# Kernel tuning notes

Measured on AMD Instinct MI355X. Metric: run time of the kernel, lower is better.

The kernel has to match this reference:

```python
import jax, jax.numpy as jnp
import numpy as np

N_EMBD = 1024
N_HEAD = 16
HEAD_DIM = N_EMBD // N_HEAD
B, S = 4, 1024


def setup_inputs() -> dict:
    key = jax.random.key(0)
    k1, k2, k3 = jax.random.split(key, 3)
    scale = 0.02
    return {
        "x": jax.random.normal(k1, (B, S, N_EMBD), dtype=jnp.float32),
        "Wqkv": jax.random.normal(k2, (N_EMBD, 3 * N_EMBD), dtype=jnp.float32) * scale,
        "bqkv": jnp.zeros((3 * N_EMBD,), dtype=jnp.float32),
        "Wproj": jax.random.normal(k3, (N_EMBD, N_EMBD), dtype=jnp.float32) * scale,
        "bproj": jnp.zeros((N_EMBD,), dtype=jnp.float32),
    }


def reference(x, Wqkv, bqkv, Wproj, bproj):
    b, s, e = x.shape
    qkv = x @ Wqkv + bqkv  # (b, s, 3e)
    q, k, v = jnp.split(qkv, 3, axis=-1)
    # (b, h, s, d)
    q = q.reshape(b, s, N_HEAD, HEAD_DIM).transpose(0, 2, 1, 3)
    k = k.reshape(b, s, N_HEAD, HEAD_DIM).transpose(0, 2, 1, 3)
    v = v.reshape(b, s, N_HEAD, HEAD_DIM).transpose(0, 2, 1, 3)
    scores = jnp.einsum("bhqd,bhkd->bhqk", q, k) / jnp.sqrt(
        jnp.asarray(HEAD_DIM, dtype=x.dtype)
    )
    causal = jnp.tril(jnp.ones((s, s), dtype=bool))  # (s, s)
    scores = jnp.where(causal[None, None, :, :], scores, jnp.asarray(-jnp.inf, dtype=scores.dtype))
    attn = jax.nn.softmax(scores, axis=-1)
    out = jnp.einsum("bhqk,bhkd->bhqd", attn, v)
    out = out.transpose(0, 2, 1, 3).reshape(b, s, e)
    return out @ Wproj + bproj
```

## Files before the change

### kernel.cpp

```cpp
#include <hip/hip_runtime.h>

#define S_LEN 1024
#define EMB   1024
#define NH    16
#define HD    64
#define BATCH 4
#define M_TOT 4096
#define QSZ   (BATCH * NH * S_LEN * HD)

typedef __attribute__((ext_vector_type(4))) float  f32x4;
typedef __attribute__((ext_vector_type(8))) __bf16 bf16x8;

__device__ __forceinline__ unsigned short f2bf(float f) {
  union { float f; unsigned u; } a; a.f = f;
  unsigned r = a.u + 0x7fffu + ((a.u >> 16) & 1u);
  return (unsigned short)(r >> 16);
}

__device__ __forceinline__ float fexp2(float x) {
#if __has_builtin(__builtin_amdgcn_exp2f)
  return __builtin_amdgcn_exp2f(x);
#else
  return exp2f(x);
#endif
}

__global__ void cvt_bf16(const float4* __restrict__ in, ushort4* __restrict__ out, int n4) {
  int i = blockIdx.x * blockDim.x + threadIdx.x;
  if (i >= n4) return;
  float4 v = in[i];
  ushort4 o;
  o.x = f2bf(v.x); o.y = f2bf(v.y); o.z = f2bf(v.z); o.w = f2bf(v.w);
  out[i] = o;
}

__global__ void cvt_transpose(const float* __restrict__ in, unsigned short* __restrict__ out,
                              int K, int N) {
  __shared__ unsigned short tile[32][33];
  int n0 = blockIdx.x * 32, k0 = blockIdx.y * 32;
  int tx = threadIdx.x, ty = threadIdx.y;
  #pragma unroll
  for (int r = ty; r < 32; r += 8)
    tile[r][tx] = f2bf(in[(size_t)(k0 + r) * N + n0 + tx]);
  __syncthreads();
  #pragma unroll
  for (int r = ty; r < 32; r += 8)
    out[(size_t)(n0 + r) * K + k0 + tx] = tile[tx][r];
}

template<int EPI>
__global__ __launch_bounds__(512, 4) void gemm_tile(
    const unsigned short* __restrict__ A,
    const unsigned short* __restrict__ Bt,
    const float* __restrict__ bias,
    void* __restrict__ outp,
    int K, int Nout)
{
  __shared__ alignas(16) char smem[65536];
  const int m0 = blockIdx.x * 128, n0 = blockIdx.y * 128;
  const int t = threadIdx.x;
  const int wid = t >> 6, lane = t & 63;
  const int wm = wid >> 2, wn = wid & 3;
  const int lr = lane & 15, lg = lane >> 4;
  const int nkt = K >> 6;

  f32x4 acc[4][2] = {};

  auto STAGE = [&](int b, int kt) {
    const int k0 = kt << 6;
    #pragma unroll
    for (int l = 0; l < 2; ++l) {
      const int L = l * 8192 + t * 16;
      const int row = L >> 7, c = (L >> 4) & 7;
      const int ce = (c ^ (row & 7)) << 3;
      const unsigned short* gA = A  + (size_t)(m0 + row) * K + k0 + ce;
      const unsigned short* gB = Bt + (size_t)(n0 + row) * K + k0 + ce;
      __builtin_amdgcn_global_load_lds(
          (const __attribute__((address_space(1))) unsigned int*)gA,
          (__attribute__((address_space(3))) unsigned int*)(smem + b * 32768 + L),
          16, 0, 0);
      __builtin_amdgcn_global_load_lds(
          (const __attribute__((address_space(1))) unsigned int*)gB,
          (__attribute__((address_space(3))) unsigned int*)(smem + b * 32768 + 16384 + L),
          16, 0, 0);
    }
  };

  STAGE(0, 0);

  for (int kt = 0; kt < nkt; ++kt) {
    const int cur = kt & 1;
    if (kt + 1 < nkt) {
      STAGE(cur ^ 1, kt + 1);
      asm volatile("s_waitcnt vmcnt(4)" ::: "memory");
    } else {
      asm volatile("s_waitcnt vmcnt(0)" ::: "memory");
    }
    __builtin_amdgcn_s_barrier();
    asm volatile("" ::: "memory");

    const char* Ab = smem + cur * 32768;
    const char* Bb = Ab + 16384;
    bf16x8 af[4][2], bfr[2][2];
    #pragma unroll
    for (int i = 0; i < 4; ++i)
      #pragma unroll
      for (int kk = 0; kk < 2; ++kk) {
        const int row = wm * 64 + i * 16 + lr;
        af[i][kk] = *(const bf16x8*)(Ab + row * 128 + (((kk * 4 + lg) ^ (row & 7)) << 4));
      }
    #pragma unroll
    for (int j = 0; j < 2; ++j)
      #pragma unroll
      for (int kk = 0; kk < 2; ++kk) {
        const int row = wn * 32 + j * 16 + lr;
        bfr[j][kk] = *(const bf16x8*)(Bb + row * 128 + (((kk * 4 + lg) ^ (row & 7)) << 4));
      }
    __builtin_amdgcn_s_setprio(1);
    #pragma unroll
    for (int i = 0; i < 4; ++i)
      #pragma unroll
      for (int j = 0; j < 2; ++j)
        #pragma unroll
        for (int kk = 0; kk < 2; ++kk)
          acc[i][j] = __builtin_amdgcn_mfma_f32_16x16x32_bf16(af[i][kk], bfr[j][kk], acc[i][j], 0, 0, 0);
    __builtin_amdgcn_s_setprio(0);

    asm volatile("s_waitcnt lgkmcnt(0)" ::: "memory");
    __builtin_amdgcn_s_barrier();
  }

  if (EPI == 0) {
    unsigned short* O = (unsigned short*)outp;
    const int sec = n0 >> 10;
    if (sec < 2) {
      #pragma unroll
      for (int i = 0; i < 4; ++i)
        #pragma unroll
        for (int j = 0; j < 2; ++j) {
          const int col = n0 + wn * 32 + j * 16 + lr;
          const float bv = bias[col];
          const int cc = col & 1023, h = cc >> 6, d = cc & 63;
          #pragma unroll
          for (int r = 0; r < 4; ++r) {
            const int row = m0 + wm * 64 + i * 16 + lg * 4 + r;
            float v = acc[i][j][r] + bv;
            if (sec == 0) v *= 0.18033688f;
            const int bb = row >> 10, ss = row & 1023;
            O[(size_t)sec * QSZ + (((size_t)(bb * NH + h) * S_LEN + ss) * HD + d)] = f2bf(v);
          }
        }
    } else {
      unsigned short* T = (unsigned short*)smem;
      #pragma unroll
      for (int i = 0; i < 4; ++i)
        #pragma unroll
        for (int j = 0; j < 2; ++j) {
          const int ci = wn * 32 + j * 16 + lr;
          const float bv = bias[n0 + ci];
          union { ushort4 s4; __bf16 b[4]; } pk;
          #pragma unroll
          for (int r = 0; r < 4; ++r) pk.b[r] = (__bf16)(acc[i][j][r] + bv);
          *(ushort4*)(T + ci * 136 + wm * 64 + i * 16 + lg * 4) = pk.s4;
        }
      __syncthreads();
      const int ci = t >> 2, part = t & 3;
      const int cc = (n0 - 2048) + ci;
      const int h = cc >> 6, d = cc & 63;
      const int bb2 = m0 >> 10, sbase = m0 & 1023;
      unsigned short* dst = O + 2ull * QSZ +
          ((size_t)(bb2 * NH + h) * HD + d) * S_LEN + sbase;
      #pragma unroll
      for (int u = 0; u < 4; ++u) {
        const int spos = part * 32 + u * 8;
        *(bf16x8*)(dst + spos) = *(const bf16x8*)(T + ci * 136 + spos);
      }
    }
  } else {
    float* Of = (float*)outp;
    #pragma unroll
    for (int i = 0; i < 4; ++i)
      #pragma unroll
      for (int j = 0; j < 2; ++j) {
        const int col = n0 + wn * 32 + j * 16 + lr;
        const float bv = bias[col];
        #pragma unroll
        for (int r = 0; r < 4; ++r) {
          const int row = m0 + wm * 64 + i * 16 + lg * 4 + r;
          Of[(size_t)row * (size_t)Nout + col] = acc[i][j][r] + bv;
        }
      }
  }
}

__device__ __forceinline__ void group_tile(
    const bf16x8 (&kf)[8], const bf16x8 (&vf)[8], const bf16x8 (&qf)[2],
    int kt, int q0, bool diag, int lr, int lg,
    float& m, float& lp, f32x4 (&o)[4])
{
  f32x4 sacc[4] = {};
  __builtin_amdgcn_s_setprio(1);
  #pragma unroll
  for (int nt = 0; nt < 4; ++nt)
    #pragma unroll
    for (int kk = 0; kk < 2; ++kk)
      sacc[nt] = __builtin_amdgcn_mfma_f32_16x16x32_bf16(kf[nt * 2 + kk], qf[kk], sacc[nt], 0, 0, 0);
  __builtin_amdgcn_s_setprio(0);

  float p[16];
  if (diag) {
    const int q = q0 + lr;
    #pragma unroll
    for (int nt = 0; nt < 4; ++nt)
      #pragma unroll
      for (int r = 0; r < 4; ++r) {
        int k = kt * 64 + nt * 16 + lg * 4 + r;
        p[nt * 4 + r] = (k > q) ? -1e30f : sacc[nt][r];
      }
  } else {
    #pragma unroll
    for (int nt = 0; nt < 4; ++nt)
      #pragma unroll
      for (int r = 0; r < 4; ++r)
        p[nt * 4 + r] = sacc[nt][r];
  }

  float r8[8], r4[4];
  #pragma unroll
  for (int i = 0; i < 8; ++i) r8[i] = fmaxf(p[i], p[i + 8]);
  #pragma unroll
  for (int i = 0; i < 4; ++i) r4[i] = fmaxf(r8[i], r8[i + 4]);
  float pm = fmaxf(fmaxf(r4[0], r4[1]), fmaxf(r4[2], r4[3]));
  if (__any(pm > m + 11.5f)) {
    float px = fmaxf(pm, __shfl_xor(pm, 16, 64));
    px = fmaxf(px, __shfl_xor(px, 32, 64));
    float mn = fmaxf(m, px);
    float fs = fexp2(m - mn);
    lp *= fs;
    #pragma unroll
    for (int dt = 0; dt < 4; ++dt)
      #pragma unroll
      for (int r = 0; r < 4; ++r) o[dt][r] *= fs;
    m = mn;
  }
  #pragma unroll
  for (int i = 0; i < 16; ++i) p[i] = fexp2(p[i] - m);

  float s8[8], s4[4];
  #pragma unroll
  for (int i = 0; i < 8; ++i) s8[i] = p[i] + p[i + 8];
  #pragma unroll
  for (int i = 0; i < 4; ++i) s4[i] = s8[i] + s8[i + 4];
  lp += (s4[0] + s4[1]) + (s4[2] + s4[3]);

  union { unsigned u[8]; __bf16 b[16]; } W;
  #pragma unroll
  for (int i = 0; i < 16; ++i) W.b[i] = (__bf16)p[i];

  const int dl0 = ((2 * (lg & 1) + (lg >> 1)) * 16 + lr) << 2;
  const int dl1 = ((2 * ((lg & 1) ^ 1) + (lg >> 1)) * 16 + lr) << 2;
  const bool oddlg = (lg & 1) != 0;
  const bool hb    = (lg >> 1) != 0;
  union { unsigned u[4]; bf16x8 v; } T0, T1;
  #pragma unroll
  for (int kk = 0; kk < 2; ++kk) {
    #pragma unroll
    for (int c = 0; c < 2; ++c) {
      unsigned vlo = W.u[4 * kk + c];
      unsigned vhi = W.u[4 * kk + 2 + c];
      unsigned s0 = oddlg ? vhi : vlo;
      unsigned s1 = oddlg ? vlo : vhi;
      unsigned r0 = (unsigned)__builtin_amdgcn_ds_permute(dl0, (int)s0);
      unsigned r1 = (unsigned)__builtin_amdgcn_ds_permute(dl1, (int)s1);
      unsigned* T = kk ? T1.u : T0.u;
      T[c]     = hb ? r1 : r0;
      T[2 + c] = hb ? r0 : r1;
    }
  }

  __builtin_amdgcn_s_setprio(1);
  #pragma unroll
  for (int dt = 0; dt < 4; ++dt) {
    o[dt] = __builtin_amdgcn_mfma_f32_16x16x32_bf16(vf[dt * 2 + 0], T0.v, o[dt], 0, 0, 0);
    o[dt] = __builtin_amdgcn_mfma_f32_16x16x32_bf16(vf[dt * 2 + 1], T1.v, o[dt], 0, 0, 0);
  }
  __builtin_amdgcn_s_setprio(0);
}

__device__ __forceinline__ void group_epilogue(
    const f32x4 (&o)[4], float lp, int q0, int lr, int lg,
    char* Ep, unsigned short* __restrict__ attout, int bb, int h)
{
  float l2 = lp + __shfl_xor(lp, 16, 64);
  float l4 = l2 + __shfl_xor(l2, 32, 64);
  float rl = 1.0f / l4;
  #pragma unroll
  for (int dt = 0; dt < 4; ++dt) {
    union { ushort4 s4; __bf16 b[4]; } ov;
    #pragma unroll
    for (int r = 0; r < 4; ++r) ov.b[r] = (__bf16)(o[dt][r] * rl);
    int byt = (lr * 128 + (dt * 16 + lg * 4) * 2) ^ ((lr & 7) << 4);
    *(ushort4*)(Ep + byt) = ov.s4;
  }
  asm volatile("s_waitcnt lgkmcnt(0)" ::: "memory");
  const int lane = lr + lg * 16;
  const int ql = lane >> 2, c = lane & 3;
  #pragma unroll
  for (int s = 0; s < 2; ++s) {
    int byt = (ql * 128 + (c * 16 + s * 8) * 2) ^ ((ql & 7) << 4);
    bf16x8 vrow = *(const bf16x8*)(Ep + byt);
    *(bf16x8*)(attout + (size_t)(bb * S_LEN + q0 + ql) * EMB + h * HD + c * 16 + s * 8) = vrow;
  }
}

__global__ __launch_bounds__(256, 2) void attn_fwd(
    const unsigned short* __restrict__ Q,
    const unsigned short* __restrict__ K,
    const unsigned short* __restrict__ Vt,
    unsigned short* __restrict__ attout)
{
  __shared__ alignas(16) char stage[2][16384];
  __shared__ alignas(16) char Ep_lds[4][2048];
  const int bid = blockIdx.x;
  const int bh   = ((bid & 7) << 3) | ((bid >> 3) & 7);
  const int base = bid >> 6;
  const int wv = threadIdx.x >> 6, lane = threadIdx.x & 63;
  const int pi = base * 4 + wv;
  const int lr = lane & 15, lg = lane >> 4;
  const int nkt  = 16 - base;
  const int nktl = base + 1;
  const int q0h = (63 - pi) * 16, q0l = pi * 16;
  const unsigned short* Qb = Q  + (size_t)bh * (S_LEN * HD);
  const unsigned short* Kh = K  + (size_t)bh * (S_LEN * HD);
  const unsigned short* Vh = Vt + (size_t)bh * (HD * S_LEN);
  const int bb = bh >> 4, h = bh & 15;

  auto STAGE = [&](int b, int kt) {
    char* lb = &stage[b][0];
    #pragma unroll
    for (int j = 0; j < 4; ++j) {
      if (wv < 2) {
        int L = wv * 4096 + j * 1024 + lane * 16;
        int row = L >> 7, c = (L >> 4) & 7;
        const unsigned short* src = Kh + (size_t)(kt * 64 + row) * HD + ((c ^ (row & 7)) << 3);
        __builtin_amdgcn_global_load_lds(
            (const __attribute__((address_space(1))) unsigned int*)src,
            (__attribute__((address_space(3))) unsigned int*)(lb + wv * 4096 + j * 1024),
            16, 0, 0);
      } else {
        int L = (wv - 2) * 4096 + j * 1024 + lane * 16;
        int row = L >> 7, c = (L >> 4) & 7;
        const unsigned short* src = Vh + (size_t)row * S_LEN + kt * 64 + ((c ^ (row & 7)) << 3);
        __builtin_amdgcn_global_load_lds(
            (const __attribute__((address_space(1))) unsigned int*)src,
            (__attribute__((address_space(3))) unsigned int*)(lb + 8192 + (wv - 2) * 4096 + j * 1024),
            16, 0, 0);
      }
    }
  };

  bf16x8 qfh[2], qfl[2];
  #pragma unroll
  for (int kk = 0; kk < 2; ++kk) {
    qfh[kk] = *(const bf16x8*)(Qb + (size_t)(q0h + lr) * HD + kk * 32 + lg * 8);
    qfl[kk] = *(const bf16x8*)(Qb + (size_t)(q0l + lr) * HD + kk * 32 + lg * 8);
  }

  float mh = -1e30f, lph = 0.f, ml = -1e30f, lpl = 0.f;
  f32x4 oh[4] = {}, ol[4] = {};

  STAGE(0, 0);
  asm volatile("s_waitcnt vmcnt(0)" ::: "memory");
  __syncthreads();

  for (int kt = 0; kt < nkt; ++kt) {
    const int cur = kt & 1;
    if (kt + 1 < nkt) STAGE(cur ^ 1, kt + 1);

    const char* sb = &stage[cur][0];
    bf16x8 kf[8], vf[8];
    #pragma unroll
    for (int nt = 0; nt < 4; ++nt)
      #pragma unroll
      for (int kk = 0; kk < 2; ++kk) {
        const int byt = (nt * 16 + lr) * 128 + ((((kk << 2) + lg) ^ (lr & 7)) << 4);
        kf[nt * 2 + kk] = *(const bf16x8*)(sb + byt);
        vf[nt * 2 + kk] = *(const bf16x8*)(sb + 8192 + byt);
      }

    group_tile(kf, vf, qfh, kt, q0h, kt == nkt - 1, lr, lg, mh, lph, oh);
    if (kt < nktl)
      group_tile(kf, vf, qfl, kt, q0l, kt == nktl - 1, lr, lg, ml, lpl, ol);

    asm volatile("s_waitcnt vmcnt(0)" ::: "memory");
    __syncthreads();
  }

  char* Ep = &Ep_lds[wv][0];
  group_epilogue(oh, lph, q0h, lr, lg, Ep, attout, bb, h);
  group_epilogue(ol, lpl, q0l, lr, lg, Ep, attout, bb, h);
}

extern "C" void kernel_launch(void* const* d_in, const int* in_sizes, int n_in,
                              void* d_out, int out_size, void* d_ws, size_t ws_size,
                              hipStream_t stream) {
  const float* x     = (const float*)d_in[0];
  const float* Wqkv  = (const float*)d_in[1];
  const float* bqkv  = (const float*)d_in[2];
  const float* Wproj = (const float*)d_in[3];
  const float* bproj = (const float*)d_in[4];

  unsigned short* xb     = (unsigned short*)d_ws;
  unsigned short* WqkvT  = xb     + (size_t)M_TOT * EMB;
  unsigned short* WprojT = WqkvT  + (size_t)3 * EMB * EMB;
  unsigned short* qkv    = WprojT + (size_t)EMB * EMB;
  unsigned short* att    = qkv    + 3ull * QSZ;

  cvt_bf16<<<dim3((M_TOT * EMB / 4 + 255) / 256), dim3(256), 0, stream>>>(
      (const float4*)x, (ushort4*)xb, M_TOT * EMB / 4);
  cvt_transpose<<<dim3(3 * EMB / 32, EMB / 32), dim3(32, 8), 0, stream>>>(Wqkv, WqkvT, EMB, 3 * EMB);
  cvt_transpose<<<dim3(EMB / 32, EMB / 32), dim3(32, 8), 0, stream>>>(Wproj, WprojT, EMB, EMB);

  gemm_tile<0><<<dim3(M_TOT / 128, 3 * EMB / 128), dim3(512), 0, stream>>>(
      xb, WqkvT, bqkv, (void*)qkv, EMB, 0);

  attn_fwd<<<dim3(8 * BATCH * NH), dim3(256), 0, stream>>>(
      qkv, qkv + QSZ, qkv + 2ull * QSZ, att);

  gemm_tile<1><<<dim3(M_TOT / 128, EMB / 128), dim3(512), 0, stream>>>(
      att, WprojT, bproj, d_out, EMB, EMB);
}
```

Baseline: 91.32 us.

## Fuse prep kernels, remap GEMM tiles per XCD, triple-buffer attention K/V

Merges the x conversion and both weight transposes into a single prep launch, which removes two kernel launches. The GEMMs move to a 1D grid that assigns N-tile columns by XCD so blocks on the same die share B tiles in cache. The attention kernel goes from double to triple buffering with partial vmcnt waits and raw barriers, so loads run two tiles ahead. This costs extra LDS per block, which may reduce occupancy.

```diff
diff --git a/kernel.cpp b/kernel.cpp
--- a/kernel.cpp
+++ b/kernel.cpp
@@ -25,27 +25,40 @@
 #endif
 }
 
-__global__ void cvt_bf16(const float4* __restrict__ in, ushort4* __restrict__ out, int n4) {
-  int i = blockIdx.x * blockDim.x + threadIdx.x;
-  if (i >= n4) return;
-  float4 v = in[i];
-  ushort4 o;
-  o.x = f2bf(v.x); o.y = f2bf(v.y); o.z = f2bf(v.z); o.w = f2bf(v.w);
-  out[i] = o;
-}
-
-__global__ void cvt_transpose(const float* __restrict__ in, unsigned short* __restrict__ out,
-                              int K, int N) {
+__global__ __launch_bounds__(256) void prep(
+    const float* __restrict__ x, const float* __restrict__ Wqkv,
+    const float* __restrict__ Wproj,
+    unsigned short* __restrict__ xb, unsigned short* __restrict__ WqkvT,
+    unsigned short* __restrict__ WprojT)
+{
   __shared__ unsigned short tile[32][33];
-  int n0 = blockIdx.x * 32, k0 = blockIdx.y * 32;
-  int tx = threadIdx.x, ty = threadIdx.y;
+  const int bid = blockIdx.x;
+  if (bid < 4096) {
+    const int i = bid * 256 + threadIdx.x;
+    float4 v = ((const float4*)x)[i];
+    ushort4 o;
+    o.x = f2bf(v.x); o.y = f2bf(v.y); o.z = f2bf(v.z); o.w = f2bf(v.w);
+    ((ushort4*)xb)[i] = o;
+    return;
+  }
+  const float* in; unsigned short* out; int N, n0, k0;
+  if (bid < 7168) {
+    const int b2 = bid - 4096;
+    in = Wqkv; out = WqkvT; N = 3 * EMB;
+    n0 = (b2 % 96) * 32; k0 = (b2 / 96) * 32;
+  } else {
+    const int b3 = bid - 7168;
+    in = Wproj; out = WprojT; N = EMB;
+    n0 = (b3 % 32) * 32; k0 = (b3 / 32) * 32;
+  }
+  const int tx = threadIdx.x & 31, ty = threadIdx.x >> 5;
   #pragma unroll
   for (int r = ty; r < 32; r += 8)
     tile[r][tx] = f2bf(in[(size_t)(k0 + r) * N + n0 + tx]);
   __syncthreads();
   #pragma unroll
   for (int r = ty; r < 32; r += 8)
-    out[(size_t)(n0 + r) * K + k0 + tx] = tile[tx][r];
+    out[(size_t)(n0 + r) * EMB + k0 + tx] = tile[tx][r];
 }
 
 template<int EPI>
@@ -54,10 +67,13 @@
     const unsigned short* __restrict__ Bt,
     const float* __restrict__ bias,
     void* __restrict__ outp,
-    int K, int Nout)
+    int K, int Nout, int nbx)
 {
   __shared__ alignas(16) char smem[65536];
-  const int m0 = blockIdx.x * 128, n0 = blockIdx.y * 128;
+  const int bid = blockIdx.x;
+  const int xcd = bid & 7, idx = bid >> 3;
+  const int m0 = (idx % nbx) * 128;
+  const int n0 = (xcd + 8 * (idx / nbx)) * 128;
   const int t = threadIdx.x;
   const int wid = t >> 6, lane = t & 63;
   const int wm = wid >> 2, wn = wid & 3;
@@ -319,7 +335,7 @@
     const unsigned short* __restrict__ Vt,
     unsigned short* __restrict__ attout)
 {
-  __shared__ alignas(16) char stage[2][16384];
+  __shared__ alignas(16) char stage[3][16384];
   __shared__ alignas(16) char Ep_lds[4][2048];
   const int bid = blockIdx.x;
   const int bh   = ((bid & 7) << 3) | ((bid >> 3) & 7);
@@ -370,14 +386,21 @@
   f32x4 oh[4] = {}, ol[4] = {};
 
   STAGE(0, 0);
-  asm volatile("s_waitcnt vmcnt(0)" ::: "memory");
-  __syncthreads();
+  STAGE(1, 1);
 
   for (int kt = 0; kt < nkt; ++kt) {
-    const int cur = kt & 1;
-    if (kt + 1 < nkt) STAGE(cur ^ 1, kt + 1);
-
-    const char* sb = &stage[cur][0];
+    if (kt + 2 < nkt) {
+      STAGE((kt + 2) % 3, kt + 2);
+      asm volatile("s_waitcnt vmcnt(8)" ::: "memory");
+    } else if (kt + 1 < nkt) {
+      asm volatile("s_waitcnt vmcnt(4)" ::: "memory");
+    } else {
+      asm volatile("s_waitcnt vmcnt(0)" ::: "memory");
+    }
+    __builtin_amdgcn_s_barrier();
+    asm volatile("" ::: "memory");
+
+    const char* sb = &stage[kt % 3][0];
     bf16x8 kf[8], vf[8];
     #pragma unroll
     for (int nt = 0; nt < 4; ++nt)
@@ -392,8 +415,8 @@
     if (kt < nktl)
       group_tile(kf, vf, qfl, kt, q0l, kt == nktl - 1, lr, lg, ml, lpl, ol);
 
-    asm volatile("s_waitcnt vmcnt(0)" ::: "memory");
-    __syncthreads();
+    asm volatile("s_waitcnt lgkmcnt(0)" ::: "memory");
+    __builtin_amdgcn_s_barrier();
   }
 
   char* Ep = &Ep_lds[wv][0];
@@ -416,17 +439,14 @@
   unsigned short* qkv    = WprojT + (size_t)EMB * EMB;
   unsigned short* att    = qkv    + 3ull * QSZ;
 
-  cvt_bf16<<<dim3((M_TOT * EMB / 4 + 255) / 256), dim3(256), 0, stream>>>(
-      (const float4*)x, (ushort4*)xb, M_TOT * EMB / 4);
-  cvt_transpose<<<dim3(3 * EMB / 32, EMB / 32), dim3(32, 8), 0, stream>>>(Wqkv, WqkvT, EMB, 3 * EMB);
-  cvt_transpose<<<dim3(EMB / 32, EMB / 32), dim3(32, 8), 0, stream>>>(Wproj, WprojT, EMB, EMB);
-
-  gemm_tile<0><<<dim3(M_TOT / 128, 3 * EMB / 128), dim3(512), 0, stream>>>(
-      xb, WqkvT, bqkv, (void*)qkv, EMB, 0);
+  prep<<<dim3(8192), dim3(256), 0, stream>>>(x, Wqkv, Wproj, xb, WqkvT, WprojT);
+
+  gemm_tile<0><<<dim3(768), dim3(512), 0, stream>>>(
+      xb, WqkvT, bqkv, (void*)qkv, EMB, 0, 32);
 
   attn_fwd<<<dim3(8 * BATCH * NH), dim3(256), 0, stream>>>(
       qkv, qkv + QSZ, qkv + 2ull * QSZ, att);
 
-  gemm_tile<1><<<dim3(M_TOT / 128, EMB / 128), dim3(512), 0, stream>>>(
-      att, WprojT, bproj, d_out, EMB, EMB);
-}
+  gemm_tile<1><<<dim3(256), dim3(512), 0, stream>>>(
+      att, WprojT, bproj, d_out, EMB, EMB, 32);
+}
```

Result: no change. 89.66 us (-1.8%).
